# Kernel optimization log

Hardware: AMD Instinct MI355X
Metric: run time of the kernel (lower is better)

Reference implementation:

```python
import jax, jax.numpy as jnp
import numpy as np

R, N, B, S = 20, 4096, 16, 256          # relations, total nodes, graphs, nodes per graph
DIN, HID, H = 512, 128, 4               # in_dim, hidden_dim, num_heads
D = HID * H                              # flattened node-feature width (=512)
E = 16384                                # edges per relation
NEG_SLOPE = 0.2


def _gat(h, src, dst, W, al, ar, b):
    # DGL GATConv, eval mode (dropout off), identity residual (in == H*out), allow_zero_in_degree
    z = (h @ W).reshape(N, H, HID)                        # [N,H,Dh]
    el = (z * al).sum(-1)                                 # [N,H]
    er = (z * ar).sum(-1)                                 # [N,H]
    e = jax.nn.leaky_relu(el[src] + er[dst], NEG_SLOPE)   # [E,H]
    m = jax.ops.segment_max(e, dst, num_segments=N)       # per-dst max (edge softmax)
    ex = jnp.exp(e - m[dst])
    den = jax.ops.segment_sum(ex, dst, num_segments=N)
    alpha = ex / den[dst]                                 # [E,H]
    agg = jax.ops.segment_sum(alpha[..., None] * z[src], dst, num_segments=N)
    return agg + h.reshape(N, H, HID) + b, alpha


def _rgat_conv(h, src, dst, W, al, ar, b):
    # HeteroGraphConv with aggregate='mean' over R relations; scan keeps memory flat
    def body(acc, xs):
        s, d, Wr, alr, arr, br = xs
        out, alpha = _gat(h, s, d, Wr, alr, arr, br)
        return acc + out, alpha.mean(-1)                  # attention meaned over heads -> [E]
    acc, attn = jax.lax.scan(body, jnp.zeros((N, H, HID), h.dtype), (src, dst, W, al, ar, b))
    return acc / R, attn                                  # [N,H,Dh], [R,E]


def setup_inputs() -> dict:
    key = jax.random.key(0)
    ks = jax.random.split(key, 24)
    f32 = jnp.float32
    p = lambda k, shape: jax.random.normal(k, shape, f32) * 0.05
    z = lambda shape: jnp.zeros(shape, f32)
    return {
        'feat': jax.random.normal(ks[0], (N, DIN), f32),
        'hyp_emb': jax.random.normal(ks[1], (B, D), f32),
        'edge_src': jax.random.randint(ks[2], (R, E), 0, N),
        'edge_dst': jax.random.randint(ks[3], (R, E), 0, N),
        'W1': p(ks[4], (R, DIN, H * HID)), 'al1': p(ks[5], (R, H, HID)), 'ar1': p(ks[6], (R, H, HID)), 'b1': z((R, H, HID)),
        'W2': p(ks[7], (R, D, H * HID)), 'al2': p(ks[8], (R, H, HID)), 'ar2': p(ks[9], (R, H, HID)), 'b2': z((R, H, HID)),
        'Wq': p(ks[10], (D, D)), 'bq': z(D), 'Wk': p(ks[11], (D, D)), 'bk': z(D),
        'Wv': p(ks[12], (D, D)), 'bv': z(D), 'Wo': p(ks[13], (D, D)), 'bo': z(D),
        'Wn1': p(ks[14], (2 * D, HID)), 'bn1': z(HID), 'Wn2': p(ks[15], (HID, 2)), 'bn2': z(2),
    }


def reference(feat, hyp_emb, edge_src, edge_dst,
              W1, al1, ar1, b1, W2, al2, ar2, b2,
              Wq, bq, Wk, bk, Wv, bv, Wo, bo, Wn1, bn1, Wn2, bn2):
    # --- RGAT (rgat_generation) layer 1 + attention weights ---
    h1, attn = _rgat_conv(feat, edge_src, edge_dst, W1, al1, ar1, b1)
    h1 = jax.nn.elu(h1.reshape(N, D))
    # --- layer 2 ---
    h2, _ = _rgat_conv(h1, edge_src, edge_dst, W2, al2, ar2, b2)
    feats = h2.reshape(N, D)
    # --- node importance: scatter-add edge attention onto dst nodes, summed over etypes ---
    imp = jax.ops.segment_sum(attn.reshape(-1), edge_dst.reshape(-1), num_segments=N)
    feats_p = feats.reshape(B, S, D)                      # uniform graphs: split+pad == reshape
    weighted = feats_p * imp.reshape(B, S)[..., None]
    # --- MultiheadAttention(embed=D, heads=4): query = hyp_emb broadcast to all S positions ---
    Hm, Dm = 4, D // 4
    q = (hyp_emb @ Wq + bq).reshape(B, Hm, 1, Dm)         # identical query at every position
    k = (feats_p @ Wk + bk).reshape(B, S, Hm, Dm).transpose(0, 2, 1, 3)
    v = (feats_p @ Wv + bv).reshape(B, S, Hm, Dm).transpose(0, 2, 1, 3)
    scores = jnp.einsum('bhqd,bhkd->bhqk', q, k) / jnp.sqrt(jnp.float32(Dm))
    a = jax.nn.softmax(scores, axis=-1)                   # [B,Hm,1,S]
    ctx = jnp.einsum('bhqk,bhkd->bhqd', a, v).reshape(B, 1, D)
    attn_out = jnp.broadcast_to(ctx @ Wo + bo, (B, S, D))
    # --- node classifier on concat(weighted feats, attention output) ---
    combined = jnp.concatenate([weighted, attn_out], axis=-1).reshape(N, 2 * D)
    node_logits = jax.nn.relu(combined @ Wn1 + bn1) @ Wn2 + bn2
    return node_logits, attn
```

## Files before the change

kernel.cpp:

```cpp
#include <hip/hip_runtime.h>
#include <hip/hip_bf16.h>
#include <math.h>

#define NREL 20
#define NN   4096
#define NE   16384
#define DF   512
#define NHD  4
#define DHH  128
#define NB   16
#define NS   256

typedef __attribute__((ext_vector_type(8))) __bf16 bf16x8;
typedef __attribute__((ext_vector_type(4))) float f32x4;
typedef __attribute__((ext_vector_type(2))) float f32x2;

struct f8 { unsigned char b; };

__device__ inline float bf2f(unsigned short u) {
    union { float f; unsigned int i; } c; c.i = ((unsigned int)u) << 16; return c.f;
}
__device__ inline unsigned short f2bu(float f) {
    union { __hip_bfloat16 b; unsigned short u; } c; c.b = __float2bfloat16(f); return c.u;
}
__device__ inline void storeOut(float* p, float v) { *p = v; }
__device__ inline void storeOut(__hip_bfloat16* p, float v) { *p = __float2bfloat16(v); }

__device__ inline void load_lds16(const __hip_bfloat16* g, __hip_bfloat16* l) {
    __builtin_amdgcn_global_load_lds(
        (const __attribute__((address_space(1))) unsigned int*)(const void*)g,
        (__attribute__((address_space(3))) unsigned int*)(void*)l, 16, 0, 0);
}

__device__ inline int kswz(int f, int row) { return f ^ (((row) & 7) << 3); }

__global__ __launch_bounds__(256) void prep_kernel(
    const float* __restrict__ feat, unsigned short* __restrict__ featbf,
    const float* __restrict__ b1, const float* __restrict__ b2,
    const float* __restrict__ bk, const float* __restrict__ bv,
    float* __restrict__ bsum1, float* __restrict__ bsum2,
    float* __restrict__ bkv, int* __restrict__ cnt, float* __restrict__ imp)
{
    int blk = blockIdx.x, t = threadIdx.x;
    if (blk < 1024) {
        int idx = blk * 256 + t;
        int row = idx >> 6;
        int f = (idx & 63) * 8;
        int fs = kswz(f, row);
        const float4* ip = (const float4*)&feat[(size_t)row * DF + f];
        float4 v0 = ip[0], v1 = ip[1];
        union { unsigned short u[8]; uint4 q; } o;
        o.u[0] = f2bu(v0.x); o.u[1] = f2bu(v0.y); o.u[2] = f2bu(v0.z); o.u[3] = f2bu(v0.w);
        o.u[4] = f2bu(v1.x); o.u[5] = f2bu(v1.y); o.u[6] = f2bu(v1.z); o.u[7] = f2bu(v1.w);
        *(uint4*)(featbf + (size_t)row * DF + fs) = o.q;
    } else if (blk == 1024) {
        #pragma unroll
        for (int rep = 0; rep < 2; ++rep) {
            int f = t + rep * 256;
            float s1 = 0.f, s2 = 0.f;
            #pragma unroll
            for (int r = 0; r < NREL; ++r) { s1 += b1[r * DF + f]; s2 += b2[r * DF + f]; }
            bsum1[f] = s1; bsum2[f] = s2;
        }
        for (int i = t; i < NN; i += 256) imp[i] = 0.f;
    } else if (blk == 1025) {
        #pragma unroll
        for (int j = 0; j < 4; ++j) {
            int f = t + j * 256;
            bkv[f] = (f < DF) ? bk[f] : bv[f - DF];
        }
    } else {
        int idx = (blk - 1026) * 256 + t;
        cnt[idx] = 0;
    }
}

__global__ void count_kernel(const int* __restrict__ dst, int* __restrict__ cnt) {
    int idx = blockIdx.x * 256 + threadIdx.x;
    int r = idx / NE;
    atomicAdd(&cnt[r * NN + dst[idx]], 1);
}

__global__ void scan_kernel(const int* __restrict__ cnt, int* __restrict__ rowptr,
                            int* __restrict__ woff, int* __restrict__ rowptr2,
                            int* __restrict__ croff) {
    int r = blockIdx.x;
    int t = threadIdx.x;
    __shared__ int sums[1024];
    int v[4]; int local = 0;
    if (r < NREL) {
        #pragma unroll
        for (int j = 0; j < 4; ++j) { v[j] = cnt[r * NN + t * 4 + j]; local += v[j]; }
    } else {
        #pragma unroll
        for (int j = 0; j < 4; ++j) {
            int s = 0;
            for (int rel = 0; rel < NREL; ++rel) {
                croff[rel * NN + t * 4 + j] = s;
                s += cnt[rel * NN + t * 4 + j];
            }
            v[j] = s; local += s;
        }
    }
    sums[t] = local;
    __syncthreads();
    for (int off = 1; off < 1024; off <<= 1) {
        int x = (t >= off) ? sums[t - off] : 0;
        __syncthreads();
        sums[t] += x;
        __syncthreads();
    }
    int run = (t == 0) ? 0 : sums[t - 1];
    if (r < NREL) {
        #pragma unroll
        for (int j = 0; j < 4; ++j) {
            rowptr[r * (NN + 1) + t * 4 + j] = run;
            woff[r * NN + t * 4 + j] = run;
            run += v[j];
        }
        if (t == 1023) rowptr[r * (NN + 1) + NN] = run;
    } else {
        #pragma unroll
        for (int j = 0; j < 4; ++j) { rowptr2[t * 4 + j] = run; run += v[j]; }
        if (t == 1023) rowptr2[NN] = run;
    }
}

__global__ void fill_kernel(const int* __restrict__ dst, const int* __restrict__ src,
                            int* __restrict__ woff, int* __restrict__ srcCSR,
                            int* __restrict__ eidCSR) {
    int idx = blockIdx.x * 256 + threadIdx.x;
    int r = idx / NE; int e = idx % NE;
    int pos = atomicAdd(&woff[r * NN + dst[idx]], 1);
    srcCSR[r * NE + pos] = src[idx];
    eidCSR[r * NE + pos] = e;
}

__global__ __launch_bounds__(256) void transw_kernel(
    const float* __restrict__ W, __hip_bfloat16* __restrict__ Wt, int K, int N)
{
    int r = blockIdx.z;
    __shared__ float t[32][33];
    int k0 = blockIdx.x * 32, n0 = blockIdx.y * 32;
    int tx = threadIdx.x % 32, ty = threadIdx.x / 32;
    #pragma unroll
    for (int kk = ty; kk < 32; kk += 8)
        t[kk][tx] = W[((size_t)r * K + k0 + kk) * N + n0 + tx];
    __syncthreads();
    #pragma unroll
    for (int nn = ty; nn < 32; nn += 8) {
        int row = n0 + nn;
        Wt[((size_t)r * N + row) * K + kswz(k0 + tx, row)] = __float2bfloat16(t[tx][nn]);
    }
}

__global__ __launch_bounds__(256) void transw2_kernel(
    const float* __restrict__ W1, const float* __restrict__ W2,
    const float* __restrict__ Wk, const float* __restrict__ Wv,
    __hip_bfloat16* __restrict__ Wt1, __hip_bfloat16* __restrict__ Wt2,
    __hip_bfloat16* __restrict__ WtKV)
{
    int z = blockIdx.z;
    const float* Wsrc; __hip_bfloat16* Wdst;
    if (z < NREL)           { Wsrc = W1 + (size_t)z * DF * DF;          Wdst = Wt1 + (size_t)z * DF * DF; }
    else if (z < 2 * NREL)  { Wsrc = W2 + (size_t)(z - NREL) * DF * DF; Wdst = Wt2 + (size_t)(z - NREL) * DF * DF; }
    else if (z == 2 * NREL) { Wsrc = Wk;                                Wdst = WtKV; }
    else                    { Wsrc = Wv;                                Wdst = WtKV + (size_t)DF * DF; }
    __shared__ float t[32][33];
    int k0 = blockIdx.x * 32, n0 = blockIdx.y * 32;
    int tx = threadIdx.x % 32, ty = threadIdx.x / 32;
    #pragma unroll
    for (int kk = ty; kk < 32; kk += 8)
        t[kk][tx] = Wsrc[(size_t)(k0 + kk) * DF + n0 + tx];
    __syncthreads();
    #pragma unroll
    for (int nn = ty; nn < 32; nn += 8) {
        int row = n0 + nn;
        Wdst[(size_t)row * DF + kswz(k0 + tx, row)] = __float2bfloat16(t[tx][nn]);
    }
}

__global__ __launch_bounds__(512) void zgemm8(
    const __hip_bfloat16* __restrict__ A,
    const __hip_bfloat16* __restrict__ BtAll,
    unsigned char* __restrict__ Zall,
    const float* __restrict__ al, const float* __restrict__ ar,
    float* __restrict__ el, float* __restrict__ er)
{
    const int r = blockIdx.z;
    const __hip_bfloat16* Bt = BtAll + (size_t)r * DF * DF;
    unsigned char* Z = Zall + (size_t)r * NN * DF;
    const int rowBase = blockIdx.y * 256;
    const int colBase = blockIdx.x * 256;
    __shared__ __hip_bfloat16 As[2][256][64];
    __shared__ __hip_bfloat16 Bs[2][256][64];
    const int tid = threadIdx.x;
    const int w = tid >> 6, l = tid & 63;
    const int wr = w >> 2, wc = w & 3;
    const int m15 = l & 15, q = l >> 4;
    const int swr = m15 & 7;

    const __hip_bfloat16* Ag = A + (size_t)(rowBase + (tid >> 3)) * DF + (tid & 7) * 8;
    const __hip_bfloat16* Bg = Bt + (size_t)(colBase + (tid >> 3)) * DF + (tid & 7) * 8;
    __hip_bfloat16* AsT = &As[0][0][0] + tid * 8;
    __hip_bfloat16* BsT = &Bs[0][0][0] + tid * 8;

#define STAGE_A(buf, half, kt) do { \
        const __hip_bfloat16* s_ = Ag + (size_t)((half) * 128) * DF + (kt) * 64; \
        __hip_bfloat16* d_ = AsT + (buf) * 16384 + (half) * 8192; \
        load_lds16(s_, d_); \
        load_lds16(s_ + (size_t)64 * DF, d_ + 4096); } while (0)
#define STAGE_B(buf, half, kt) do { \
        const __hip_bfloat16* s_ = Bg + (size_t)((half) * 128) * DF + (kt) * 64; \
        __hip_bfloat16* d_ = BsT + (buf) * 16384 + (half) * 8192; \
        load_lds16(s_, d_); \
        load_lds16(s_ + (size_t)64 * DF, d_ + 4096); } while (0)

    f32x4 acc[8][4];
    #pragma unroll
    for (int i = 0; i < 8; ++i)
        #pragma unroll
        for (int j = 0; j < 4; ++j) acc[i][j] = (f32x4){0.f, 0.f, 0.f, 0.f};

    const int NT = DF / 64;
    STAGE_A(0, 0, 0); STAGE_A(0, 1, 0); STAGE_B(0, 0, 0); STAGE_B(0, 1, 0);
    STAGE_A(1, 0, 1); STAGE_A(1, 1, 1);
    asm volatile("s_waitcnt vmcnt(4)" ::: "memory");
    __builtin_amdgcn_s_barrier();
    __builtin_amdgcn_sched_barrier(0);

    bf16x8 a0[8], a1[8], b0[4], b1[4];
    for (int kt = 0; kt < NT; ++kt) {
        const int buf = kt & 1, obuf = buf ^ 1;
        #pragma unroll
        for (int i = 0; i < 8; ++i)
            a0[i] = *(const bf16x8*)&As[buf][wr * 128 + i * 16 + m15][(q ^ swr) * 8];
        #pragma unroll
        for (int j = 0; j < 4; ++j)
            b0[j] = *(const bf16x8*)&Bs[buf][wc * 64 + j * 16 + m15][(q ^ swr) * 8];
        if (kt + 1 < NT) STAGE_B(obuf, 0, kt + 1);
        __builtin_amdgcn_s_barrier();
        asm volatile("s_waitcnt lgkmcnt(0)" ::: "memory");
        __builtin_amdgcn_sched_barrier(0);
        __builtin_amdgcn_s_setprio(1);
        #pragma unroll
        for (int i = 0; i < 4; ++i)
            #pragma unroll
            for (int j = 0; j < 4; ++j)
                acc[i][j] = __builtin_amdgcn_mfma_f32_16x16x32_bf16(a0[i], b0[j], acc[i][j], 0, 0, 0);
        __builtin_amdgcn_s_setprio(0);
        __builtin_amdgcn_s_barrier();
        #pragma unroll
        for (int i = 0; i < 8; ++i)
            a1[i] = *(const bf16x8*)&As[buf][wr * 128 + i * 16 + m15][((4 + q) ^ swr) * 8];
        if (kt + 1 < NT) STAGE_B(obuf, 1, kt + 1);
        __builtin_amdgcn_s_barrier();
        asm volatile("s_waitcnt lgkmcnt(0)" ::: "memory");
        __builtin_amdgcn_sched_barrier(0);
        __builtin_amdgcn_s_setprio(1);
        #pragma unroll
        for (int i = 4; i < 8; ++i)
            #pragma unroll
            for (int j = 0; j < 4; ++j)
                acc[i][j] = __builtin_amdgcn_mfma_f32_16x16x32_bf16(a0[i], b0[j], acc[i][j], 0, 0, 0);
        __builtin_amdgcn_s_setprio(0);
        __builtin_amdgcn_s_barrier();
        #pragma unroll
        for (int j = 0; j < 4; ++j)
            b1[j] = *(const bf16x8*)&Bs[buf][wc * 64 + j * 16 + m15][((4 + q) ^ swr) * 8];
        if (kt + 2 < NT) STAGE_A(buf, 0, kt + 2);
        __builtin_amdgcn_s_barrier();
        asm volatile("s_waitcnt lgkmcnt(0)" ::: "memory");
        __builtin_amdgcn_sched_barrier(0);
        __builtin_amdgcn_s_setprio(1);
        #pragma unroll
        for (int i = 0; i < 4; ++i)
            #pragma unroll
            for (int j = 0; j < 4; ++j)
                acc[i][j] = __builtin_amdgcn_mfma_f32_16x16x32_bf16(a1[i], b1[j], acc[i][j], 0, 0, 0);
        __builtin_amdgcn_s_setprio(0);
        __builtin_amdgcn_s_barrier();
        if (kt + 2 < NT) STAGE_A(buf, 1, kt + 2);
        __builtin_amdgcn_s_barrier();
        __builtin_amdgcn_s_setprio(1);
        #pragma unroll
        for (int i = 4; i < 8; ++i)
            #pragma unroll
            for (int j = 0; j < 4; ++j)
                acc[i][j] = __builtin_amdgcn_mfma_f32_16x16x32_bf16(a1[i], b1[j], acc[i][j], 0, 0, 0);
        __builtin_amdgcn_s_setprio(0);
        if (kt + 2 < NT) { asm volatile("s_waitcnt vmcnt(4)" ::: "memory"); }
        else             { asm volatile("s_waitcnt vmcnt(0)" ::: "memory"); }
        __builtin_amdgcn_s_barrier();
        __builtin_amdgcn_sched_barrier(0);
    }
#undef STAGE_A
#undef STAGE_B

    unsigned char* cbuf = (unsigned char*)&As[0][0][0];
    #pragma unroll
    for (int i = 0; i < 8; ++i)
        #pragma unroll
        for (int j = 0; j < 4; ++j) {
            int colL = wc * 64 + j * 16 + m15;
            #pragma unroll
            for (int reg = 0; reg < 4; ++reg) {
                int rowL = wr * 128 + i * 16 + q * 4 + reg;
                unsigned int pk = __builtin_amdgcn_cvt_pk_fp8_f32(
                    acc[i][j][reg], acc[i][j][reg], 0, false);
                cbuf[rowL * 256 + colL] = (unsigned char)(pk & 0xFF);
            }
        }
    __syncthreads();
    {
        int rowL = tid >> 1, colL = (tid & 1) * 128;
        const uint4* src = (const uint4*)&cbuf[rowL * 256 + colL];
        uint4* dst = (uint4*)(Z + (size_t)(rowBase + rowL) * DF + colBase + colL);
        #pragma unroll
        for (int x = 0; x < 8; ++x) dst[x] = src[x];
    }

    float alv[4], arv[4];
    #pragma unroll
    for (int j = 0; j < 4; ++j) {
        int col = colBase + wc * 64 + j * 16 + m15;
        alv[j] = al[r * DF + col];
        arv[j] = ar[r * DF + col];
    }
    float pe[8][4], pr[8][4];
    #pragma unroll
    for (int i = 0; i < 8; ++i)
        #pragma unroll
        for (int reg = 0; reg < 4; ++reg) {
            float se = 0.f, sr = 0.f;
            #pragma unroll
            for (int j = 0; j < 4; ++j) {
                se += acc[i][j][reg] * alv[j];
                sr += acc[i][j][reg] * arv[j];
            }
            pe[i][reg] = se; pr[i][reg] = sr;
        }
    #pragma unroll
    for (int off = 1; off < 16; off <<= 1)
        #pragma unroll
        for (int i = 0; i < 8; ++i)
            #pragma unroll
            for (int reg = 0; reg < 4; ++reg) {
                pe[i][reg] += __shfl_xor(pe[i][reg], off);
                pr[i][reg] += __shfl_xor(pr[i][reg], off);
            }
    float* eP = (float*)&Bs[0][0][0];
    float* rP = eP + 1024;
    if (m15 == 0) {
        int hh = wc >> 1, strip = wc & 1;
        #pragma unroll
        for (int i = 0; i < 8; ++i)
            #pragma unroll
            for (int reg = 0; reg < 4; ++reg) {
                int rowL = wr * 128 + i * 16 + q * 4 + reg;
                eP[(hh * 256 + rowL) * 2 + strip] = pe[i][reg];
                rP[(hh * 256 + rowL) * 2 + strip] = pr[i][reg];
            }
    }
    __syncthreads();
    {
        int rowL = tid & 255, hh = tid >> 8;
        int head = (colBase >> 7) + hh;
        size_t idx = ((size_t)r * NN + rowBase + rowL) * NHD + head;
        el[idx] = eP[(hh * 256 + rowL) * 2] + eP[(hh * 256 + rowL) * 2 + 1];
        er[idx] = rP[(hh * 256 + rowL) * 2] + rP[(hh * 256 + rowL) * 2 + 1];
    }
}

template <typename OutT, bool RELU, bool FUSE, bool SPLITK = false>
__global__ __launch_bounds__(256) void mfma_gemm(
    const __hip_bfloat16* __restrict__ A,
    const __hip_bfloat16* __restrict__ BtAll,
    const float* __restrict__ bias, int biasStride,
    OutT* __restrict__ Call, int M, int N, int K, int lda,
    const float* __restrict__ al, const float* __restrict__ ar,
    float* __restrict__ el, float* __restrict__ er)
{
    int r = blockIdx.z;
    const __hip_bfloat16* Bt;
    int koff;
    if (SPLITK) { Bt = BtAll;                         koff = r * K; }
    else        { Bt = BtAll + (size_t)r * N * lda;   koff = 0; }
    OutT* C = Call + (size_t)r * M * N;
    const int rowBase = blockIdx.y * 128;
    const int colBase = blockIdx.x * 128;
    __shared__ __hip_bfloat16 As[128 * 64];
    __shared__ __hip_bfloat16 Bs[128 * 64];
    const int tid = threadIdx.x;
    const int w = tid >> 6, l = tid & 63;
    const int wr = w >> 1, wc = w & 1;
    const int m15 = l & 15, q = l >> 4;
    const int sRow = tid >> 3;
    const int sChk = tid & 7;
    const __hip_bfloat16* Ag = A + (size_t)(rowBase + sRow) * lda + koff + sChk * 8;
    const __hip_bfloat16* Bg = Bt + (size_t)(colBase + sRow) * lda + koff + sChk * 8;
    __hip_bfloat16* Asl = As + tid * 8;
    __hip_bfloat16* Bsl = Bs + tid * 8;
    const int swr = m15 & 7;

    f32x4 acc[4][4];
    #pragma unroll
    for (int i = 0; i < 4; ++i)
        #pragma unroll
        for (int j = 0; j < 4; ++j) acc[i][j] = (f32x4){0.f, 0.f, 0.f, 0.f};

    for (int k0 = 0; k0 < K; k0 += 64) {
        #pragma unroll
        for (int c = 0; c < 4; ++c) {
            load_lds16(Ag + (size_t)c * 32 * lda + k0, Asl + c * 2048);
            load_lds16(Bg + (size_t)c * 32 * lda + k0, Bsl + c * 2048);
        }
        __syncthreads();
        #pragma unroll
        for (int g = 0; g < 2; ++g) {
            bf16x8 a[4], b[4];
            #pragma unroll
            for (int i = 0; i < 4; ++i)
                a[i] = *(const bf16x8*)&As[(wr * 64 + i * 16 + m15) * 64 + ((g * 4 + q) ^ swr) * 8];
            #pragma unroll
            for (int j = 0; j < 4; ++j)
                b[j] = *(const bf16x8*)&Bs[(wc * 64 + j * 16 + m15) * 64 + ((g * 4 + q) ^ swr) * 8];
            #pragma unroll
            for (int i = 0; i < 4; ++i)
                #pragma unroll
                for (int j = 0; j < 4; ++j)
                    acc[i][j] = __builtin_amdgcn_mfma_f32_16x16x32_bf16(a[i], b[j], acc[i][j], 0, 0, 0);
        }
        __syncthreads();
    }

    if constexpr (sizeof(OutT) == 1) {
        unsigned char* cbuf = (unsigned char*)As;
        #pragma unroll
        for (int i = 0; i < 4; ++i)
            #pragma unroll
            for (int j = 0; j < 4; ++j) {
                int colL = wc * 64 + j * 16 + m15;
                #pragma unroll
                for (int reg = 0; reg < 4; ++reg) {
                    int rowL = wr * 64 + i * 16 + q * 4 + reg;
                    unsigned int pk = __builtin_amdgcn_cvt_pk_fp8_f32(
                        acc[i][j][reg], acc[i][j][reg], 0, false);
                    cbuf[rowL * 128 + colL] = (unsigned char)(pk & 0xFF);
                }
            }
        __syncthreads();
        int rowL = tid >> 1, colL = (tid & 1) * 64;
        const uint4* src = (const uint4*)&cbuf[rowL * 128 + colL];
        uint4* dst = (uint4*)((unsigned char*)C + (size_t)(rowBase + rowL) * N
                              + colBase + colL);
        #pragma unroll
        for (int x = 0; x < 4; ++x) dst[x] = src[x];
    } else {
        #pragma unroll
        for (int i = 0; i < 4; ++i) {
            #pragma unroll
            for (int j = 0; j < 4; ++j) {
                int col = colBase + wc * 64 + j * 16 + m15;
                float bv = bias ? bias[r * biasStride + col] : 0.f;
                #pragma unroll
                for (int reg = 0; reg < 4; ++reg) {
                    int row = rowBase + wr * 64 + i * 16 + q * 4 + reg;
                    float v = acc[i][j][reg] + bv;
                    if (RELU) v = fmaxf(v, 0.f);
                    storeOut(&C[(size_t)row * N + col], v);
                }
            }
        }
    }

    if (FUSE) {
        float alv[4], arv[4];
        #pragma unroll
        for (int j = 0; j < 4; ++j) {
            int col = colBase + wc * 64 + j * 16 + m15;
            alv[j] = al[r * DF + col];
            arv[j] = ar[r * DF + col];
        }
        float pe[4][4], pr[4][4];
        #pragma unroll
        for (int i = 0; i < 4; ++i)
            #pragma unroll
            for (int reg = 0; reg < 4; ++reg) {
                float se = 0.f, sr = 0.f;
                #pragma unroll
                for (int j = 0; j < 4; ++j) {
                    se += acc[i][j][reg] * alv[j];
                    sr += acc[i][j][reg] * arv[j];
                }
                pe[i][reg] = se; pr[i][reg] = sr;
            }
        #pragma unroll
        for (int off = 1; off < 16; off <<= 1)
            #pragma unroll
            for (int i = 0; i < 4; ++i)
                #pragma unroll
                for (int reg = 0; reg < 4; ++reg) {
                    pe[i][reg] += __shfl_xor(pe[i][reg], off);
                    pr[i][reg] += __shfl_xor(pr[i][reg], off);
                }
        float* eP = (float*)Bs;
        float* rP = eP + 256;
        if (m15 == 0) {
            #pragma unroll
            for (int i = 0; i < 4; ++i)
                #pragma unroll
                for (int reg = 0; reg < 4; ++reg) {
                    int rowL = wr * 64 + i * 16 + q * 4 + reg;
                    eP[rowL * 2 + wc] = pe[i][reg];
                    rP[rowL * 2 + wc] = pr[i][reg];
                }
        }
        __syncthreads();
        if (tid < 128) {
            int head = colBase >> 7;
            size_t idx = ((size_t)r * NN + rowBase + tid) * NHD + head;
            el[idx] = eP[tid * 2] + eP[tid * 2 + 1];
            er[idx] = rP[tid * 2] + rP[tid * 2 + 1];
        }
    }
}

template <typename OutT>
__global__ __launch_bounds__(256) void gemm_kernel(
    const float* __restrict__ A, const float* __restrict__ Bm,
    const float* __restrict__ bias, OutT* __restrict__ C,
    int M, int K, int Nn)
{
    int r = blockIdx.z;
    const float* B = Bm + (size_t)r * K * Nn;
    OutT* Cr = C + (size_t)r * M * Nn;
    int rowBase = blockIdx.y * 64;
    int colBase = blockIdx.x * 64;
    __shared__ float As[64][17];
    __shared__ float Bs[16][64];
    int tid = threadIdx.x;
    int tx = tid % 16, ty = tid / 16;
    float acc[4][4] = {};
    int aRow = tid / 4, aK4 = (tid % 4) * 4;
    int bK = tid / 16, bN4 = (tid % 16) * 4;
    for (int k0 = 0; k0 < K; k0 += 16) {
        int gRow = rowBase + aRow;
        float4 av = make_float4(0.f, 0.f, 0.f, 0.f);
        if (gRow < M) av = *(const float4*)(A + (size_t)gRow * K + k0 + aK4);
        As[aRow][aK4 + 0] = av.x; As[aRow][aK4 + 1] = av.y;
        As[aRow][aK4 + 2] = av.z; As[aRow][aK4 + 3] = av.w;
        float4 bv = *(const float4*)(B + (size_t)(k0 + bK) * Nn + colBase + bN4);
        *(float4*)&Bs[bK][bN4] = bv;
        __syncthreads();
        #pragma unroll
        for (int k = 0; k < 16; ++k) {
            float a[4], b[4];
            #pragma unroll
            for (int i = 0; i < 4; ++i) a[i] = As[ty * 4 + i][k];
            #pragma unroll
            for (int j = 0; j < 4; ++j) b[j] = Bs[k][tx * 4 + j];
            #pragma unroll
            for (int i = 0; i < 4; ++i)
                #pragma unroll
                for (int j = 0; j < 4; ++j) acc[i][j] += a[i] * b[j];
        }
        __syncthreads();
    }
    #pragma unroll
    for (int i = 0; i < 4; ++i) {
        int gRow = rowBase + ty * 4 + i;
        if (gRow >= M) continue;
        #pragma unroll
        for (int j = 0; j < 4; ++j) {
            int gCol = colBase + tx * 4 + j;
            float v = acc[i][j];
            if (bias) v += bias[gCol];
            storeOut(&Cr[(size_t)gRow * Nn + gCol], v);
        }
    }
}

__global__ __launch_bounds__(256) void alpha_kernel(
    const float* __restrict__ el, const float* __restrict__ er,
    const int* __restrict__ rowptr, const int* __restrict__ rowptr2,
    const int* __restrict__ croff, const int* __restrict__ srcCSR,
    const int* __restrict__ eidCSR,
    float* __restrict__ alphaPk, int* __restrict__ srcPk,
    float* __restrict__ attn, float* __restrict__ imp)
{
    int t = blockIdx.x * 256 + threadIdx.x;
    int r = t / NN, n = t % NN;
    int start = rowptr[r * (NN + 1) + n];
    int d = rowptr[r * (NN + 1) + n + 1] - start;
    if (d == 0) return;
    int pbase = rowptr2[n] + croff[r * NN + n];
    float4 er4 = *(const float4*)&er[((size_t)r * NN + n) * NHD];
    float4 den = make_float4(0.f, 0.f, 0.f, 0.f);
    for (int j = 0; j < d; ++j) {
        int s = srcCSR[r * NE + start + j];
        float4 el4 = *(const float4*)&el[((size_t)r * NN + s) * NHD];
        float v0 = el4.x + er4.x; v0 = v0 > 0.f ? v0 : 0.2f * v0;
        float v1 = el4.y + er4.y; v1 = v1 > 0.f ? v1 : 0.2f * v1;
        float v2 = el4.z + er4.z; v2 = v2 > 0.f ? v2 : 0.2f * v2;
        float v3 = el4.w + er4.w; v3 = v3 > 0.f ? v3 : 0.2f * v3;
        float4 e4 = make_float4(__expf(v0), __expf(v1), __expf(v2), __expf(v3));
        den.x += e4.x; den.y += e4.y; den.z += e4.z; den.w += e4.w;
        *(float4*)&alphaPk[(size_t)(pbase + j) * 4] = e4;
        srcPk[pbase + j] = r * NN + s;
    }
    float4 inv = make_float4(1.f / den.x, 1.f / den.y, 1.f / den.z, 1.f / den.w);
    float impLoc = 0.f;
    for (int j = 0; j < d; ++j) {
        float4 a4 = *(const float4*)&alphaPk[(size_t)(pbase + j) * 4];
        a4.x *= inv.x; a4.y *= inv.y; a4.z *= inv.z; a4.w *= inv.w;
        *(float4*)&alphaPk[(size_t)(pbase + j) * 4] = a4;
        if (attn) {
            float a = 0.25f * (a4.x + a4.y + a4.z + a4.w);
            attn[r * NE + eidCSR[r * NE + start + j]] = a;
            impLoc += a;
        }
    }
    if (attn) atomicAdd(&imp[n], impLoc);
}

__global__ __launch_bounds__(256) void aggc_kernel(
    const unsigned char* __restrict__ Z,
    const int* __restrict__ rowptr2, const int* __restrict__ srcPk,
    const float* __restrict__ alphaPk, const float* __restrict__ bsum,
    const float* __restrict__ hin, float* __restrict__ hout,
    __hip_bfloat16* __restrict__ hout_bf, int applyElu)
{
    int n = blockIdx.x;
    int w = threadIdx.x >> 6, lane = threadIdx.x & 63;
    int h = lane >> 4;
    int base = rowptr2[n];
    int deg = rowptr2[n + 1] - base;
    float acc[8] = {};
    if (deg > 0) {
        int i = w * 4;
        int zz[4]; float aa[4];
        #pragma unroll
        for (int j = 0; j < 4; ++j) {
            int idx = i + j; int cidx = idx < deg ? idx : deg - 1;
            zz[j] = srcPk[base + cidx];
            aa[j] = (idx < deg) ? alphaPk[(size_t)(base + cidx) * 4 + h] : 0.f;
        }
        while (i < deg) {
            int cz[4]; float ca[4];
            #pragma unroll
            for (int j = 0; j < 4; ++j) { cz[j] = zz[j]; ca[j] = aa[j]; }
            int ni = i + 16;
            #pragma unroll
            for (int j = 0; j < 4; ++j) {
                int idx = ni + j; int cidx = idx < deg ? idx : deg - 1;
                zz[j] = srcPk[base + cidx];
                aa[j] = (idx < deg) ? alphaPk[(size_t)(base + cidx) * 4 + h] : 0.f;
            }
            uint2 raw[4];
            #pragma unroll
            for (int j = 0; j < 4; ++j)
                raw[j] = *(const uint2*)&Z[(size_t)cz[j] * DF + lane * 8];
            #pragma unroll
            for (int j = 0; j < 4; ++j) {
                f32x2 f01 = __builtin_amdgcn_cvt_pk_f32_fp8((int)raw[j].x, false);
                f32x2 f23 = __builtin_amdgcn_cvt_pk_f32_fp8((int)raw[j].x, true);
                f32x2 f45 = __builtin_amdgcn_cvt_pk_f32_fp8((int)raw[j].y, false);
                f32x2 f67 = __builtin_amdgcn_cvt_pk_f32_fp8((int)raw[j].y, true);
                acc[0] += ca[j] * f01.x; acc[1] += ca[j] * f01.y;
                acc[2] += ca[j] * f23.x; acc[3] += ca[j] * f23.y;
                acc[4] += ca[j] * f45.x; acc[5] += ca[j] * f45.y;
                acc[6] += ca[j] * f67.x; acc[7] += ca[j] * f67.y;
            }
            i = ni;
        }
    }
    __shared__ float red[4][DF];
    #pragma unroll
    for (int j = 0; j < 8; ++j) red[w][lane * 8 + j] = acc[j];
    __syncthreads();
    const float invR = 1.0f / NREL;
    const int sw = (n & 7) << 3;
    int f = threadIdx.x;
    #pragma unroll
    for (int rep = 0; rep < 2; ++rep, f += 256) {
        float v = red[0][f] + red[1][f] + red[2][f] + red[3][f];
        v = (v + bsum[f]) * invR + hin[(size_t)n * DF + f];
        if (applyElu) v = v > 0.f ? v : expm1f(v);
        hout[(size_t)n * DF + f] = v;
        hout_bf[(size_t)n * DF + (f ^ sw)] = __float2bfloat16(v);
    }
}

__global__ __launch_bounds__(256) void mha_scores(
    const float* __restrict__ q, const float* __restrict__ k,
    float* __restrict__ scores)
{
    int b = blockIdx.x;
    int w = threadIdx.x >> 6, lane = threadIdx.x & 63;
    int s = blockIdx.y * 4 + w;
    const float4* qp = (const float4*)&q[(size_t)b * DF + lane * 8];
    const float4* kp = (const float4*)&k[((size_t)(b * NS + s)) * DF + lane * 8];
    float4 q0 = qp[0], q1 = qp[1];
    float4 k0 = kp[0], k1 = kp[1];
    float p = q0.x * k0.x + q0.y * k0.y + q0.z * k0.z + q0.w * k0.w
            + q1.x * k1.x + q1.y * k1.y + q1.z * k1.z + q1.w * k1.w;
    #pragma unroll
    for (int off = 1; off < 16; off <<= 1) p += __shfl_xor(p, off);
    if ((lane & 15) == 0) {
        int h = lane >> 4;
        scores[((size_t)(b * NHD + h)) * NS + s] = p * 0.08838834764831845f;
    }
}

__global__ __launch_bounds__(256) void mha_ctx(
    const float* __restrict__ scores, const float* __restrict__ v,
    float* __restrict__ ctx)
{
    int b = blockIdx.x, h = blockIdx.y;
    int t = threadIdx.x;
    int lane = t & 63, w = t >> 6;
    __shared__ float a_s[NS];
    __shared__ float wred[8];
    float sv = scores[((size_t)(b * NHD + h)) * NS + t];
    float mx = sv;
    #pragma unroll
    for (int off = 1; off < 64; off <<= 1) mx = fmaxf(mx, __shfl_xor(mx, off));
    if (lane == 0) wred[w] = mx;
    __syncthreads();
    mx = fmaxf(fmaxf(wred[0], wred[1]), fmaxf(wred[2], wred[3]));
    float e = __expf(sv - mx);
    float sum = e;
    #pragma unroll
    for (int off = 1; off < 64; off <<= 1) sum += __shfl_xor(sum, off);
    if (lane == 0) wred[4 + w] = sum;
    __syncthreads();
    sum = wred[4] + wred[5] + wred[6] + wred[7];
    a_s[t] = e * (1.0f / sum);
    __syncthreads();
    int d = t & 127, half = t >> 7;
    float acc = 0.f;
    const float* vp = &v[((size_t)(b * NS + half * 128)) * DF + h * DHH + d];
    #pragma unroll 4
    for (int i = 0; i < 128; ++i)
        acc += a_s[half * 128 + i] * vp[(size_t)i * DF];
    __shared__ float red[256];
    red[t] = acc;
    __syncthreads();
    if (t < 128) ctx[(size_t)b * DF + h * DHH + t] = red[t] + red[t + 128];
}

__global__ __launch_bounds__(256) void combined_kernel(
    const float* __restrict__ feats, const float* __restrict__ imp,
    const float* __restrict__ abuf, __hip_bfloat16* __restrict__ comb)
{
    int n = blockIdx.x;
    int t = threadIdx.x;
    int b = n >> 8;
    float im = imp[n];
    const int sw = (n & 7) << 3;
    #pragma unroll
    for (int rep = 0; rep < 4; ++rep) {
        int f = t + rep * 256;
        float v = (f < DF) ? feats[(size_t)n * DF + f] * im
                           : abuf[(size_t)b * DF + (f - DF)];
        comb[(size_t)n * (2 * DF) + (f ^ sw)] = __float2bfloat16(v);
    }
}

__global__ __launch_bounds__(256) void cls2_kernel(
    const float* __restrict__ hidden4, const float* __restrict__ bn1,
    const float* __restrict__ Wn2, const float* __restrict__ bn2,
    float* __restrict__ out)
{
    __shared__ float w2[256];
    __shared__ float b1s[128];
    int t = threadIdx.x;
    w2[t] = Wn2[t];
    if (t < 128) b1s[t] = bn1[t];
    __syncthreads();
    int n = blockIdx.x * 256 + t;
    const float* hp = &hidden4[(size_t)n * 128];
    const size_t ps = (size_t)NN * 128;
    float p0 = bn2[0], p1 = bn2[1];
    #pragma unroll 4
    for (int kk = 0; kk < 128; ++kk) {
        float hv = hp[kk] + hp[ps + kk] + hp[2 * ps + kk] + hp[3 * ps + kk] + b1s[kk];
        hv = fmaxf(hv, 0.f);
        p0 += hv * w2[kk * 2 + 0];
        p1 += hv * w2[kk * 2 + 1];
    }
    out[n * 2 + 0] = p0;
    out[n * 2 + 1] = p1;
}

extern "C" void kernel_launch(void* const* d_in, const int* in_sizes, int n_in,
                              void* d_out, int out_size, void* d_ws, size_t ws_size,
                              hipStream_t stream) {
    const float* feat = (const float*)d_in[0];
    const float* hyp  = (const float*)d_in[1];
    const int*   esrc = (const int*)d_in[2];
    const int*   edst = (const int*)d_in[3];
    const float* W1   = (const float*)d_in[4];
    const float* al1  = (const float*)d_in[5];
    const float* ar1  = (const float*)d_in[6];
    const float* b1   = (const float*)d_in[7];
    const float* W2   = (const float*)d_in[8];
    const float* al2  = (const float*)d_in[9];
    const float* ar2  = (const float*)d_in[10];
    const float* b2   = (const float*)d_in[11];
    const float* Wq = (const float*)d_in[12]; const float* bq = (const float*)d_in[13];
    const float* Wk = (const float*)d_in[14]; const float* bk = (const float*)d_in[15];
    const float* Wv = (const float*)d_in[16]; const float* bv = (const float*)d_in[17];
    const float* Wo = (const float*)d_in[18]; const float* bo = (const float*)d_in[19];
    const float* Wn1 = (const float*)d_in[20]; const float* bn1 = (const float*)d_in[21];
    const float* Wn2 = (const float*)d_in[22]; const float* bn2 = (const float*)d_in[23];

    char* ws = (char*)d_ws;
    size_t off = 0;
    auto alloc = [&](size_t bytes) -> void* {
        void* p = ws + off;
        off += (bytes + 255) & ~(size_t)255;
        return p;
    };
    unsigned char* Z = (unsigned char*)alloc((size_t)NREL * NN * DF);
    float* el     = (float*)alloc((size_t)NREL * NN * NHD * 4);
    float* er     = (float*)alloc((size_t)NREL * NN * NHD * 4);
    int* rowptr   = (int*)alloc((size_t)NREL * (NN + 1) * 4);
    int* rowptr2  = (int*)alloc((size_t)(NN + 1) * 4);
    int* woff     = (int*)alloc((size_t)NREL * NN * 4);
    int* srcCSR   = (int*)alloc((size_t)NREL * NE * 4);
    int* eidCSR   = (int*)alloc((size_t)NREL * NE * 4);
    int* cnt      = (int*)alloc((size_t)NREL * NN * 4);
    int* croff    = (int*)alloc((size_t)NREL * NN * 4);
    int* srcPk    = (int*)alloc((size_t)NREL * NE * 4);
    float* alphaPk= (float*)alloc((size_t)NREL * NE * NHD * 4);
    float* bsum1  = (float*)alloc((size_t)DF * 4);
    float* bsum2  = (float*)alloc((size_t)DF * 4);
    float* bkv    = (float*)alloc((size_t)2 * DF * 4);
    float* h1     = (float*)alloc((size_t)NN * DF * 4);
    float* feats  = (float*)alloc((size_t)NN * DF * 4);
    float* imp    = (float*)alloc((size_t)NN * 4);
    float* kvbuf  = (float*)alloc((size_t)2 * NN * DF * 4);
    float* qbuf   = (float*)alloc((size_t)NB * DF * 4);
    float* ctxb   = (float*)alloc((size_t)NB * DF * 4);
    float* abuf   = (float*)alloc((size_t)NB * DF * 4);
    float* scoresb= (float*)alloc((size_t)NB * NHD * NS * 4);
    float* hidden4= (float*)alloc((size_t)4 * NN * 128 * 4);
    __hip_bfloat16* featbf  = (__hip_bfloat16*)alloc((size_t)NN * DF * 2);
    __hip_bfloat16* h1bf    = (__hip_bfloat16*)alloc((size_t)NN * DF * 2);
    __hip_bfloat16* featsbf = (__hip_bfloat16*)alloc((size_t)NN * DF * 2);
    __hip_bfloat16* combbf  = (__hip_bfloat16*)alloc((size_t)NN * 2 * DF * 2);
    __hip_bfloat16* Wt1 = (__hip_bfloat16*)alloc((size_t)NREL * DF * DF * 2);
    __hip_bfloat16* Wt2 = (__hip_bfloat16*)alloc((size_t)NREL * DF * DF * 2);
    __hip_bfloat16* WtKV = (__hip_bfloat16*)alloc((size_t)2 * DF * DF * 2);
    __hip_bfloat16* Wn1t = (__hip_bfloat16*)alloc((size_t)(2 * DF) * 128 * 2);
    if (off > ws_size) return;

    float* logits = (float*)d_out;
    float* attn   = (float*)d_out + (size_t)NN * 2;
    float* kbuf = kvbuf;
    float* vbuf = kvbuf + (size_t)NN * DF;

    prep_kernel<<<1026 + NREL * NN / 256, 256, 0, stream>>>(
        feat, (unsigned short*)featbf, b1, b2, bk, bv, bsum1, bsum2, bkv, cnt, imp);

    count_kernel<<<NREL * NE / 256, 256, 0, stream>>>(edst, cnt);
    scan_kernel<<<NREL + 1, 1024, 0, stream>>>(cnt, rowptr, woff, rowptr2, croff);
    fill_kernel<<<NREL * NE / 256, 256, 0, stream>>>(edst, esrc, woff, srcCSR, eidCSR);

    transw2_kernel<<<dim3(DF / 32, DF / 32, 2 * NREL + 2), 256, 0, stream>>>(
        W1, W2, Wk, Wv, Wt1, Wt2, WtKV);
    transw_kernel<<<dim3(2 * DF / 32, 128 / 32, 1), 256, 0, stream>>>(Wn1, Wn1t, 2 * DF, 128);

    zgemm8<<<dim3(DF / 256, NN / 256, NREL), 512, 0, stream>>>(
        featbf, Wt1, Z, al1, ar1, el, er);
    alpha_kernel<<<NREL * NN / 256, 256, 0, stream>>>(
        el, er, rowptr, rowptr2, croff, srcCSR, eidCSR, alphaPk, srcPk, attn, imp);
    aggc_kernel<<<NN, 256, 0, stream>>>(Z, rowptr2, srcPk, alphaPk, bsum1,
                                        feat, h1, h1bf, 1);

    zgemm8<<<dim3(DF / 256, NN / 256, NREL), 512, 0, stream>>>(
        h1bf, Wt2, Z, al2, ar2, el, er);
    alpha_kernel<<<NREL * NN / 256, 256, 0, stream>>>(
        el, er, rowptr, rowptr2, croff, srcCSR, eidCSR, alphaPk, srcPk, nullptr, nullptr);
    aggc_kernel<<<NN, 256, 0, stream>>>(Z, rowptr2, srcPk, alphaPk, bsum2,
                                        h1, feats, featsbf, 0);

    mfma_gemm<float, false, false><<<dim3(DF / 128, NN / 128, 2), 256, 0, stream>>>(
        featsbf, WtKV, bkv, DF, kvbuf, NN, DF, DF, DF, nullptr, nullptr, nullptr, nullptr);
    gemm_kernel<float><<<dim3(DF / 64, 1, 1), 256, 0, stream>>>(
        hyp, Wq, bq, qbuf, NB, DF, DF);
    mha_scores<<<dim3(NB, NS / 4), 256, 0, stream>>>(qbuf, kbuf, scoresb);
    mha_ctx<<<dim3(NB, NHD), 256, 0, stream>>>(scoresb, vbuf, ctxb);
    gemm_kernel<float><<<dim3(DF / 64, 1, 1), 256, 0, stream>>>(
        ctxb, Wo, bo, abuf, NB, DF, DF);

    combined_kernel<<<NN, 256, 0, stream>>>(feats, imp, abuf, combbf);
    mfma_gemm<float, false, false, true><<<dim3(1, NN / 128, 4), 256, 0, stream>>>(
        combbf, Wn1t, nullptr, 0, hidden4, NN, 128, 256, 2 * DF,
        nullptr, nullptr, nullptr, nullptr);
    cls2_kernel<<<NN / 256, 256, 0, stream>>>(hidden4, bn1, Wn2, bn2, logits);
}
```

Before: 584.7 us.

## Simplify GEMM main loop to one-barrier double-buffered schedule with full-tile prefetch

Replaces the four-phase, many-barrier interleaved K-loop with a simpler schedule. Each iteration loads all A and B fragments for the tile from LDS up front and passes one barrier. It then issues global-to-LDS staging of both A and B for tile kt+2 into the just-freed buffer and runs all 64 MFMAs back to back. This cuts barrier count and increases register pressure, since a0/a1/b0/b1 are live together, and it loses the fine-grained overlap of LDS reads with MFMA.

```diff
diff --git a/kernel.cpp b/kernel.cpp
--- a/kernel.cpp
+++ b/kernel.cpp
@@ -224,73 +224,45 @@
 
     const int NT = DF / 64;
     STAGE_A(0, 0, 0); STAGE_A(0, 1, 0); STAGE_B(0, 0, 0); STAGE_B(0, 1, 0);
-    STAGE_A(1, 0, 1); STAGE_A(1, 1, 1);
-    asm volatile("s_waitcnt vmcnt(4)" ::: "memory");
+    STAGE_A(1, 0, 1); STAGE_A(1, 1, 1); STAGE_B(1, 0, 1); STAGE_B(1, 1, 1);
+    asm volatile("s_waitcnt vmcnt(8)" ::: "memory");
     __builtin_amdgcn_s_barrier();
     __builtin_amdgcn_sched_barrier(0);
 
     bf16x8 a0[8], a1[8], b0[4], b1[4];
     for (int kt = 0; kt < NT; ++kt) {
-        const int buf = kt & 1, obuf = buf ^ 1;
+        const int buf = kt & 1;
+        #pragma unroll
+        for (int i = 0; i < 8; ++i) {
+            a0[i] = *(const bf16x8*)&As[buf][wr * 128 + i * 16 + m15][(q ^ swr) * 8];
+            a1[i] = *(const bf16x8*)&As[buf][wr * 128 + i * 16 + m15][((4 + q) ^ swr) * 8];
+        }
+        #pragma unroll
+        for (int j = 0; j < 4; ++j) {
+            b0[j] = *(const bf16x8*)&Bs[buf][wc * 64 + j * 16 + m15][(q ^ swr) * 8];
+            b1[j] = *(const bf16x8*)&Bs[buf][wc * 64 + j * 16 + m15][((4 + q) ^ swr) * 8];
+        }
+        asm volatile("s_waitcnt lgkmcnt(0)" ::: "memory");
+        __builtin_amdgcn_s_barrier();
+        __builtin_amdgcn_sched_barrier(0);
+        if (kt + 2 < NT) {
+            STAGE_A(buf, 0, kt + 2); STAGE_A(buf, 1, kt + 2);
+            STAGE_B(buf, 0, kt + 2); STAGE_B(buf, 1, kt + 2);
+        }
+        __builtin_amdgcn_s_setprio(1);
         #pragma unroll
         for (int i = 0; i < 8; ++i)
-            a0[i] = *(const bf16x8*)&As[buf][wr * 128 + i * 16 + m15][(q ^ swr) * 8];
-        #pragma unroll
-        for (int j = 0; j < 4; ++j)
-            b0[j] = *(const bf16x8*)&Bs[buf][wc * 64 + j * 16 + m15][(q ^ swr) * 8];
-        if (kt + 1 < NT) STAGE_B(obuf, 0, kt + 1);
-        __builtin_amdgcn_s_barrier();
-        asm volatile("s_waitcnt lgkmcnt(0)" ::: "memory");
-        __builtin_amdgcn_sched_barrier(0);
-        __builtin_amdgcn_s_setprio(1);
-        #pragma unroll
-        for (int i = 0; i < 4; ++i)
             #pragma unroll
             for (int j = 0; j < 4; ++j)
                 acc[i][j] = __builtin_amdgcn_mfma_f32_16x16x32_bf16(a0[i], b0[j], acc[i][j], 0, 0, 0);
-        __builtin_amdgcn_s_setprio(0);
-        __builtin_amdgcn_s_barrier();
         #pragma unroll
         for (int i = 0; i < 8; ++i)
-            a1[i] = *(const bf16x8*)&As[buf][wr * 128 + i * 16 + m15][((4 + q) ^ swr) * 8];
-        if (kt + 1 < NT) STAGE_B(obuf, 1, kt + 1);
-        __builtin_amdgcn_s_barrier();
-        asm volatile("s_waitcnt lgkmcnt(0)" ::: "memory");
-        __builtin_amdgcn_sched_barrier(0);
-        __builtin_amdgcn_s_setprio(1);
-        #pragma unroll
-        for (int i = 4; i < 8; ++i)
-            #pragma unroll
-            for (int j = 0; j < 4; ++j)
-                acc[i][j] = __builtin_amdgcn_mfma_f32_16x16x32_bf16(a0[i], b0[j], acc[i][j], 0, 0, 0);
-        __builtin_amdgcn_s_setprio(0);
-        __builtin_amdgcn_s_barrier();
-        #pragma unroll
-        for (int j = 0; j < 4; ++j)
-            b1[j] = *(const bf16x8*)&Bs[buf][wc * 64 + j * 16 + m15][((4 + q) ^ swr) * 8];
-        if (kt + 2 < NT) STAGE_A(buf, 0, kt + 2);
-        __builtin_amdgcn_s_barrier();
-        asm volatile("s_waitcnt lgkmcnt(0)" ::: "memory");
-        __builtin_amdgcn_sched_barrier(0);
-        __builtin_amdgcn_s_setprio(1);
-        #pragma unroll
-        for (int i = 0; i < 4; ++i)
             #pragma unroll
             for (int j = 0; j < 4; ++j)
                 acc[i][j] = __builtin_amdgcn_mfma_f32_16x16x32_bf16(a1[i], b1[j], acc[i][j], 0, 0, 0);
         __builtin_amdgcn_s_setprio(0);
-        __builtin_amdgcn_s_barrier();
-        if (kt + 2 < NT) STAGE_A(buf, 1, kt + 2);
-        __builtin_amdgcn_s_barrier();
-        __builtin_amdgcn_s_setprio(1);
-        #pragma unroll
-        for (int i = 4; i < 8; ++i)
-            #pragma unroll
-            for (int j = 0; j < 4; ++j)
-                acc[i][j] = __builtin_amdgcn_mfma_f32_16x16x32_bf16(a1[i], b1[j], acc[i][j], 0, 0, 0);
-        __builtin_amdgcn_s_setprio(0);
-        if (kt + 2 < NT) { asm volatile("s_waitcnt vmcnt(4)" ::: "memory"); }
-        else             { asm volatile("s_waitcnt vmcnt(0)" ::: "memory"); }
+        if (kt + 2 < NT)      { asm volatile("s_waitcnt vmcnt(8)" ::: "memory"); }
+        else if (kt + 1 < NT) { asm volatile("s_waitcnt vmcnt(0)" ::: "memory"); }
         __builtin_amdgcn_s_barrier();
         __builtin_amdgcn_sched_barrier(0);
     }
```

Measured after the change: 582.8 us. About the same (-0.3%).
